# Kernel tuning notes

Hardware: AMD Instinct MI355X
Metric: run time of the kernel (lower is better)

The kernel has to match this reference:

```python
import jax, jax.numpy as jnp
import numpy as np

B, N, C = 4, 1024, 256
E = 65536
HID = 256  # LAYERS = [256, 256, 256]

def _linear_init(key, out_dim, in_dim):
    kw, kb = jax.random.split(key)
    s = 1.0 / np.sqrt(in_dim)
    W = jax.random.uniform(kw, (out_dim, in_dim), jnp.float32, -s, s)
    b = jax.random.uniform(kb, (out_dim,), jnp.float32, -s, s)
    return W, b

def setup_inputs() -> dict:
    key = jax.random.key(0)
    ks = jax.random.split(key, 5)
    pooled_features = jax.random.normal(ks[0], (B, N, C), jnp.float32)
    edge_index = jax.random.randint(ks[1], (2, E), 0, B * N)  # [src; dst]
    W1, b1 = _linear_init(ks[2], HID, 2 * C)
    W2, b2 = _linear_init(ks[3], HID, 2 * HID)
    W3, b3 = _linear_init(ks[4], HID, 2 * HID)
    return {"pooled_features": pooled_features, "edge_index": edge_index,
            "W1": W1, "b1": b1, "W2": W2, "b2": b2, "W3": W3, "b3": b3}

def _edge_conv(x, src, dst, num_nodes, W, b):
    # PyG EdgeConv: x_j = x[src], x_i = x[dst]; msg = relu(fc([x_j - x_i, x_i]));
    # aggr='max' scatters messages onto dst nodes.
    x_i = x[dst]                                   # [E, d]
    x_j = x[src]                                   # [E, d]
    msg = jnp.concatenate([x_j - x_i, x_i], axis=-1)  # [E, 2d]
    msg = jax.nn.relu(msg @ W.T + b)               # [E, out]
    out = jax.ops.segment_max(msg, dst, num_segments=num_nodes)
    # empty segments -> -inf; PyG fills with 0, and relu messages are >= 0
    return jnp.maximum(out, 0.0)

def reference(pooled_features, edge_index, W1, b1, W2, b2, W3, b3):
    b_, n_, c_ = pooled_features.shape
    num_nodes = b_ * n_
    x = pooled_features.reshape(num_nodes, c_)
    src, dst = edge_index[0], edge_index[1]
    feats = [x]
    for W, bb in ((W1, b1), (W2, b2), (W3, b3)):
        x = _edge_conv(x, src, dst, num_nodes, W, bb)
        feats.append(x)
    related_features = jnp.concatenate(feats, axis=-1)  # [num_nodes, 1024]
    return related_features
```

## Files before the change

### kernel.cpp

```cpp
#include <hip/hip_runtime.h>


#define NODES 4096
#define EDGES 65536
#define OSTR 1024
#define DEGCAP 64

typedef __attribute__((ext_vector_type(8))) short bf16x8;
typedef __attribute__((ext_vector_type(4))) float f32x4;

__device__ __forceinline__ unsigned short f2bf(float f) {
    unsigned int x = __float_as_uint(f);
    return (unsigned short)((x + 0x7fff + ((x >> 16) & 1)) >> 16);
}
__device__ __forceinline__ float bf2f(unsigned short u) {
    return __uint_as_float(((unsigned int)u) << 16);
}

__device__ __forceinline__ void gemm_phase(int l, const short* Alds,
                                           const short* __restrict__ Wp,
                                           const float* __restrict__ bias,
                                           unsigned short* __restrict__ UWu,
                                           float* __restrict__ UWw,
                                           int b, int t) {
    const int wv = t >> 6, lane = t & 63;
    const int lm = lane & 15, kq = lane >> 4;
    const int nhalf = wv >> 3, sub = wv & 7;
    f32x4 acc0 = (f32x4){0.f, 0.f, 0.f, 0.f};
    f32x4 acc1 = (f32x4){0.f, 0.f, 0.f, 0.f};
    const short* ap = Alds + lm * 264 + kq * 8;
    const short* bp = Wp + (size_t)l * 131072
                         + (size_t)(nhalf * 256 + sub * 32 + lm) * 256 + kq * 8;
#pragma unroll
    for (int ks = 0; ks < 8; ++ks) {
        const int ko = ks * 32;
        bf16x8 a  = *(const bf16x8*)(ap + ko);
        bf16x8 q0 = *(const bf16x8*)(bp + ko);
        bf16x8 q1 = *(const bf16x8*)(bp + 16 * 256 + ko);
        acc0 = __builtin_amdgcn_mfma_f32_16x16x32_bf16(a, q0, acc0, 0, 0, 0);
        acc1 = __builtin_amdgcn_mfma_f32_16x16x32_bf16(a, q1, acc1, 0, 0, 0);
    }
    unsigned short* UW = UWu + (size_t)(l & 1) * NODES * 256;
#pragma unroll
    for (int nt2 = 0; nt2 < 2; ++nt2) {
        int nc = sub * 32 + nt2 * 16 + lm;
        f32x4 av = nt2 ? acc1 : acc0;
        if (nhalf == 0) {
#pragma unroll
            for (int p = 0; p < 4; ++p)
                UW[(size_t)(b * 16 + kq * 4 + p) * 256 + nc] = f2bf(av[p]);
        } else {
            float bc = bias[nc];
#pragma unroll
            for (int p = 0; p < 4; ++p)
                UWw[(size_t)(b * 16 + kq * 4 + p) * 256 + nc] = av[p] + bc;
        }
    }
}

__device__ __forceinline__ void edge_phase(int l,
                                           const unsigned short* __restrict__ UWu,
                                           const float* __restrict__ UWw,
                                           const int* __restrict__ cursor,
                                           const int* __restrict__ srcS,
                                           float* __restrict__ out,
                                           short* AldsW, int b, int t) {
    const int wv = t >> 6, lane = t & 63;
    const int i = b * 16 + wv;
    int deg = cursor[i]; if (deg > DEGCAP) deg = DEGCAP;
    const int beg = i * DEGCAP, end = beg + deg;
    const unsigned short* UW = UWu + (size_t)(l & 1) * NODES * 256;
    const float NEG = -3.4e38f;
    float mx0 = NEG, mx1 = NEG, mx2 = NEG, mx3 = NEG;
    int e = beg;
    for (; e + 8 <= end; e += 8) {
        int4 sa = *(const int4*)(srcS + e);
        int4 sb = *(const int4*)(srcS + e + 4);
        ushort4 v0 = *(const ushort4*)(UW + (size_t)sa.x * 256 + lane * 4);
        ushort4 v1 = *(const ushort4*)(UW + (size_t)sa.y * 256 + lane * 4);
        ushort4 v2 = *(const ushort4*)(UW + (size_t)sa.z * 256 + lane * 4);
        ushort4 v3 = *(const ushort4*)(UW + (size_t)sa.w * 256 + lane * 4);
        ushort4 v4 = *(const ushort4*)(UW + (size_t)sb.x * 256 + lane * 4);
        ushort4 v5 = *(const ushort4*)(UW + (size_t)sb.y * 256 + lane * 4);
        ushort4 v6 = *(const ushort4*)(UW + (size_t)sb.z * 256 + lane * 4);
        ushort4 v7 = *(const ushort4*)(UW + (size_t)sb.w * 256 + lane * 4);
        mx0 = fmaxf(mx0, fmaxf(fmaxf(bf2f(v0.x), bf2f(v1.x)), fmaxf(bf2f(v2.x), bf2f(v3.x))));
        mx0 = fmaxf(mx0, fmaxf(fmaxf(bf2f(v4.x), bf2f(v5.x)), fmaxf(bf2f(v6.x), bf2f(v7.x))));
        mx1 = fmaxf(mx1, fmaxf(fmaxf(bf2f(v0.y), bf2f(v1.y)), fmaxf(bf2f(v2.y), bf2f(v3.y))));
        mx1 = fmaxf(mx1, fmaxf(fmaxf(bf2f(v4.y), bf2f(v5.y)), fmaxf(bf2f(v6.y), bf2f(v7.y))));
        mx2 = fmaxf(mx2, fmaxf(fmaxf(bf2f(v0.z), bf2f(v1.z)), fmaxf(bf2f(v2.z), bf2f(v3.z))));
        mx2 = fmaxf(mx2, fmaxf(fmaxf(bf2f(v4.z), bf2f(v5.z)), fmaxf(bf2f(v6.z), bf2f(v7.z))));
        mx3 = fmaxf(mx3, fmaxf(fmaxf(bf2f(v0.w), bf2f(v1.w)), fmaxf(bf2f(v2.w), bf2f(v3.w))));
        mx3 = fmaxf(mx3, fmaxf(fmaxf(bf2f(v4.w), bf2f(v5.w)), fmaxf(bf2f(v6.w), bf2f(v7.w))));
    }
    for (; e + 4 <= end; e += 4) {
        int4 sa = *(const int4*)(srcS + e);
        ushort4 v0 = *(const ushort4*)(UW + (size_t)sa.x * 256 + lane * 4);
        ushort4 v1 = *(const ushort4*)(UW + (size_t)sa.y * 256 + lane * 4);
        ushort4 v2 = *(const ushort4*)(UW + (size_t)sa.z * 256 + lane * 4);
        ushort4 v3 = *(const ushort4*)(UW + (size_t)sa.w * 256 + lane * 4);
        mx0 = fmaxf(mx0, fmaxf(fmaxf(bf2f(v0.x), bf2f(v1.x)), fmaxf(bf2f(v2.x), bf2f(v3.x))));
        mx1 = fmaxf(mx1, fmaxf(fmaxf(bf2f(v0.y), bf2f(v1.y)), fmaxf(bf2f(v2.y), bf2f(v3.y))));
        mx2 = fmaxf(mx2, fmaxf(fmaxf(bf2f(v0.z), bf2f(v1.z)), fmaxf(bf2f(v2.z), bf2f(v3.z))));
        mx3 = fmaxf(mx3, fmaxf(fmaxf(bf2f(v0.w), bf2f(v1.w)), fmaxf(bf2f(v2.w), bf2f(v3.w))));
    }
    for (; e < end; ++e) {
        int s = srcS[e];
        ushort4 v = *(const ushort4*)(UW + (size_t)s * 256 + lane * 4);
        mx0 = fmaxf(mx0, bf2f(v.x)); mx1 = fmaxf(mx1, bf2f(v.y));
        mx2 = fmaxf(mx2, bf2f(v.z)); mx3 = fmaxf(mx3, bf2f(v.w));
    }
    float4 w4 = *(const float4*)(UWw + (size_t)i * 256 + lane * 4);
    f32x4 r;
    r[0] = fmaxf(mx0 + w4.x, 0.0f);
    r[1] = fmaxf(mx1 + w4.y, 0.0f);
    r[2] = fmaxf(mx2 + w4.z, 0.0f);
    r[3] = fmaxf(mx3 + w4.w, 0.0f);
    *(f32x4*)(out + (size_t)i * OSTR + (l + 1) * 256 + lane * 4) = r;
    if (AldsW) {
        ushort4 rb;
        rb.x = f2bf(r[0]); rb.y = f2bf(r[1]); rb.z = f2bf(r[2]); rb.w = f2bf(r[3]);
        *(ushort4*)(AldsW + wv * 264 + lane * 4) = rb;
    }
}

__global__ __launch_bounds__(256) void k_prep(const float* __restrict__ W0,
                                              const float* __restrict__ W1,
                                              const float* __restrict__ W2,
                                              short* __restrict__ Wp,
                                              int* __restrict__ cursor) {
    int tid = blockIdx.x * 256 + threadIdx.x;
    const float* Ws[3] = {W0, W1, W2};
#pragma unroll
    for (int layer = 0; layer < 3; ++layer) {
        const float* W = Ws[layer];
        int n2 = tid >> 8, c = tid & 255;
        float wv2 = (n2 < 256) ? W[n2 * 512 + c]
                               : W[(n2 - 256) * 512 + 256 + c] - W[(n2 - 256) * 512 + c];
        Wp[layer * 131072 + tid] = (short)f2bf(wv2);
    }
    if (tid < NODES) cursor[tid] = 0;
}

__global__ __launch_bounds__(1024, 4) void k_g0(const float* __restrict__ x0,
                                                const int* __restrict__ srcIdx,
                                                const int* __restrict__ dstIdx,
                                                const short* __restrict__ Wp,
                                                const float* __restrict__ B0,
                                                unsigned short* __restrict__ UWu,
                                                float* __restrict__ UWw,
                                                int* __restrict__ cursor,
                                                int* __restrict__ srcS,
                                                float* __restrict__ out) {
    __shared__ __align__(16) short Alds[16 * 264];
    const int t = threadIdx.x, b = blockIdx.x;
    const int gtid = b * 1024 + t;
    {
        int row = t >> 6, c4 = t & 63;
        f32x4 v = *((const f32x4*)x0 + (size_t)(b * 16 + row) * 64 + c4);
        ((f32x4*)out)[(size_t)(b * 16 + row) * 256 + c4] = v;
        ushort4 hb;
        hb.x = f2bf(v[0]); hb.y = f2bf(v[1]); hb.z = f2bf(v[2]); hb.w = f2bf(v[3]);
        *(ushort4*)(Alds + row * 264 + c4 * 4) = hb;
    }
    if (gtid < EDGES) {
        int d = dstIdx[gtid];
        int p = atomicAdd(&cursor[d], 1);
        if (p < DEGCAP) srcS[d * DEGCAP + p] = srcIdx[gtid];
    }
    __syncthreads();
    gemm_phase(0, Alds, Wp, B0, UWu, UWw, b, t);
}

__global__ __launch_bounds__(1024, 4) void k_eg(int l,
                                                const short* __restrict__ Wp,
                                                const float* __restrict__ biasN,
                                                unsigned short* __restrict__ UWu,
                                                float* __restrict__ UWw,
                                                const int* __restrict__ cursor,
                                                const int* __restrict__ srcS,
                                                float* __restrict__ out) {
    __shared__ __align__(16) short Alds[16 * 264];
    const int t = threadIdx.x, b = blockIdx.x;
    edge_phase(l, UWu, UWw, cursor, srcS, out, Alds, b, t);
    __syncthreads();
    gemm_phase(l + 1, Alds, Wp, biasN, UWu, UWw, b, t);
}

__global__ __launch_bounds__(1024, 4) void k_e2(const unsigned short* __restrict__ UWu,
                                                const float* __restrict__ UWw,
                                                const int* __restrict__ cursor,
                                                const int* __restrict__ srcS,
                                                float* __restrict__ out) {
    const int t = threadIdx.x, b = blockIdx.x;
    edge_phase(2, UWu, UWw, cursor, srcS, out, (short*)nullptr, b, t);
}

extern "C" void kernel_launch(void* const* d_in, const int* in_sizes, int n_in,
                              void* d_out, int out_size, void* d_ws, size_t ws_size,
                              hipStream_t stream) {
    const float* x0 = (const float*)d_in[0];
    const int* ei = (const int*)d_in[1];
    const int* srcIdx = ei;
    const int* dstIdx = ei + EDGES;
    float* out = (float*)d_out;

    char* w = (char*)d_ws;
    unsigned short* UWu = (unsigned short*)w;
    float* UWw = (float*)(w + 4194304);
    short* Wp = (short*)(w + 8388608);
    int* srcS = (int*)(w + 9175040);
    int* cursor = (int*)(w + 10223616);

    const float* W0 = (const float*)d_in[2]; const float* B0 = (const float*)d_in[3];
    const float* W1 = (const float*)d_in[4]; const float* B1 = (const float*)d_in[5];
    const float* W2 = (const float*)d_in[6]; const float* B2 = (const float*)d_in[7];

    k_prep<<<512, 256, 0, stream>>>(W0, W1, W2, Wp, cursor);
    k_g0<<<256, 1024, 0, stream>>>(x0, srcIdx, dstIdx, Wp, B0, UWu, UWw, cursor, srcS, out);
    k_eg<<<256, 1024, 0, stream>>>(0, Wp, B1, UWu, UWw, cursor, srcS, out);
    k_eg<<<256, 1024, 0, stream>>>(1, Wp, B2, UWu, UWw, cursor, srcS, out);
    k_e2<<<256, 1024, 0, stream>>>(UWu, UWw, cursor, srcS, out);
}
```

Baseline: 131.0 us.

## Fold weight prep into first kernel and bucket edges per block with LDS atomics

Removes the separate prep kernel. Layer-0 weights are now converted straight from fp32 into MFMA B-fragments held in registers, and the layer-1/2 weight packing is spread across k_g0's threads. Edge bucketing changes from global atomics on a cursor array to a per-block scan of all destination indices, using LDS atomics only for the block's own 16 nodes, so the cursor zeroing and its launch go away. The cost is that every block reads the full dst array (64K ints) and holds extra registers for the fragments. The order of sources within each bucket can also change.

```diff
diff --git a/kernel.cpp b/kernel.cpp
--- a/kernel.cpp
+++ b/kernel.cpp
@@ -15,6 +15,14 @@
 }
 __device__ __forceinline__ float bf2f(unsigned short u) {
     return __uint_as_float(((unsigned int)u) << 16);
+}
+__device__ __forceinline__ bf16x8 pack8(float4 a, float4 b) {
+    bf16x8 r;
+    r[0] = (short)f2bf(a.x); r[1] = (short)f2bf(a.y);
+    r[2] = (short)f2bf(a.z); r[3] = (short)f2bf(a.w);
+    r[4] = (short)f2bf(b.x); r[5] = (short)f2bf(b.y);
+    r[6] = (short)f2bf(b.z); r[7] = (short)f2bf(b.w);
+    return r;
 }
 
 __device__ __forceinline__ void gemm_phase(int l, const short* Alds,
@@ -58,16 +66,52 @@
     }
 }
 
+__device__ __forceinline__ void gemm_regs(int par, const bf16x8 fb[2][8],
+                                          const short* Alds,
+                                          const float* __restrict__ bias,
+                                          unsigned short* __restrict__ UWu,
+                                          float* __restrict__ UWw,
+                                          int b, int t) {
+    const int wv = t >> 6, lane = t & 63;
+    const int lm = lane & 15, kq = lane >> 4;
+    const int nhalf = wv >> 3, sub = wv & 7;
+    f32x4 acc0 = (f32x4){0.f, 0.f, 0.f, 0.f};
+    f32x4 acc1 = (f32x4){0.f, 0.f, 0.f, 0.f};
+    const short* ap = Alds + lm * 264 + kq * 8;
+#pragma unroll
+    for (int ks = 0; ks < 8; ++ks) {
+        bf16x8 a = *(const bf16x8*)(ap + ks * 32);
+        acc0 = __builtin_amdgcn_mfma_f32_16x16x32_bf16(a, fb[0][ks], acc0, 0, 0, 0);
+        acc1 = __builtin_amdgcn_mfma_f32_16x16x32_bf16(a, fb[1][ks], acc1, 0, 0, 0);
+    }
+    unsigned short* UW = UWu + (size_t)par * NODES * 256;
+#pragma unroll
+    for (int nt2 = 0; nt2 < 2; ++nt2) {
+        int nc = sub * 32 + nt2 * 16 + lm;
+        f32x4 av = nt2 ? acc1 : acc0;
+        if (nhalf == 0) {
+#pragma unroll
+            for (int p = 0; p < 4; ++p)
+                UW[(size_t)(b * 16 + kq * 4 + p) * 256 + nc] = f2bf(av[p]);
+        } else {
+            float bc = bias[nc];
+#pragma unroll
+            for (int p = 0; p < 4; ++p)
+                UWw[(size_t)(b * 16 + kq * 4 + p) * 256 + nc] = av[p] + bc;
+        }
+    }
+}
+
 __device__ __forceinline__ void edge_phase(int l,
                                            const unsigned short* __restrict__ UWu,
                                            const float* __restrict__ UWw,
-                                           const int* __restrict__ cursor,
+                                           const int* __restrict__ degG,
                                            const int* __restrict__ srcS,
                                            float* __restrict__ out,
                                            short* AldsW, int b, int t) {
     const int wv = t >> 6, lane = t & 63;
     const int i = b * 16 + wv;
-    int deg = cursor[i]; if (deg > DEGCAP) deg = DEGCAP;
+    int deg = degG[i]; if (deg > DEGCAP) deg = DEGCAP;
     const int beg = i * DEGCAP, end = beg + deg;
     const unsigned short* UW = UWu + (size_t)(l & 1) * NODES * 256;
     const float NEG = -3.4e38f;
@@ -124,37 +168,24 @@
     }
 }
 
-__global__ __launch_bounds__(256) void k_prep(const float* __restrict__ W0,
-                                              const float* __restrict__ W1,
-                                              const float* __restrict__ W2,
-                                              short* __restrict__ Wp,
-                                              int* __restrict__ cursor) {
-    int tid = blockIdx.x * 256 + threadIdx.x;
-    const float* Ws[3] = {W0, W1, W2};
-#pragma unroll
-    for (int layer = 0; layer < 3; ++layer) {
-        const float* W = Ws[layer];
-        int n2 = tid >> 8, c = tid & 255;
-        float wv2 = (n2 < 256) ? W[n2 * 512 + c]
-                               : W[(n2 - 256) * 512 + 256 + c] - W[(n2 - 256) * 512 + c];
-        Wp[layer * 131072 + tid] = (short)f2bf(wv2);
-    }
-    if (tid < NODES) cursor[tid] = 0;
-}
-
 __global__ __launch_bounds__(1024, 4) void k_g0(const float* __restrict__ x0,
                                                 const int* __restrict__ srcIdx,
                                                 const int* __restrict__ dstIdx,
-                                                const short* __restrict__ Wp,
+                                                const float* __restrict__ W0,
+                                                const float* __restrict__ W1,
+                                                const float* __restrict__ W2,
                                                 const float* __restrict__ B0,
+                                                short* __restrict__ Wp,
                                                 unsigned short* __restrict__ UWu,
                                                 float* __restrict__ UWw,
-                                                int* __restrict__ cursor,
+                                                int* __restrict__ degG,
                                                 int* __restrict__ srcS,
                                                 float* __restrict__ out) {
     __shared__ __align__(16) short Alds[16 * 264];
+    __shared__ int degL[16];
     const int t = threadIdx.x, b = blockIdx.x;
     const int gtid = b * 1024 + t;
+    if (t < 16) degL[t] = 0;
     {
         int row = t >> 6, c4 = t & 63;
         f32x4 v = *((const f32x4*)x0 + (size_t)(b * 16 + row) * 64 + c4);
@@ -163,13 +194,61 @@
         hb.x = f2bf(v[0]); hb.y = f2bf(v[1]); hb.z = f2bf(v[2]); hb.w = f2bf(v[3]);
         *(ushort4*)(Alds + row * 264 + c4 * 4) = hb;
     }
-    if (gtid < EDGES) {
-        int d = dstIdx[gtid];
-        int p = atomicAdd(&cursor[d], 1);
-        if (p < DEGCAP) srcS[d * DEGCAP + p] = srcIdx[gtid];
+    {
+        const float* W = (gtid >= 131072) ? W2 : W1;
+        int idx = gtid & 131071;
+        int n2 = idx >> 8, c = idx & 255;
+        float wv2 = (n2 < 256) ? W[n2 * 512 + c]
+                               : W[(n2 - 256) * 512 + 256 + c] - W[(n2 - 256) * 512 + c];
+        Wp[131072 + gtid] = (short)f2bf(wv2);
+    }
+    const int wv = t >> 6, lane = t & 63;
+    const int lm = lane & 15, kq = lane >> 4;
+    const int nhalf = wv >> 3, sub = wv & 7;
+    bf16x8 fb[2][8];
+    {
+        const int r0 = sub * 32 + lm;
+#pragma unroll
+        for (int rr = 0; rr < 2; ++rr) {
+            const float* rp = W0 + (size_t)(r0 + rr * 16) * 512 + kq * 8;
+#pragma unroll
+            for (int ks = 0; ks < 8; ++ks) {
+                const int ko = ks * 32;
+                if (nhalf == 0) {
+                    fb[rr][ks] = pack8(*(const float4*)(rp + ko),
+                                       *(const float4*)(rp + ko + 4));
+                } else {
+                    float4 a0 = *(const float4*)(rp + ko);
+                    float4 a1 = *(const float4*)(rp + ko + 4);
+                    float4 c0 = *(const float4*)(rp + 256 + ko);
+                    float4 c1 = *(const float4*)(rp + 256 + ko + 4);
+                    float4 d0, d1;
+                    d0.x = c0.x - a0.x; d0.y = c0.y - a0.y;
+                    d0.z = c0.z - a0.z; d0.w = c0.w - a0.w;
+                    d1.x = c1.x - a1.x; d1.y = c1.y - a1.y;
+                    d1.z = c1.z - a1.z; d1.w = c1.w - a1.w;
+                    fb[rr][ks] = pack8(d0, d1);
+                }
+            }
+        }
     }
     __syncthreads();
-    gemm_phase(0, Alds, Wp, B0, UWu, UWw, b, t);
+#pragma unroll 4
+    for (int j = 0; j < 16; ++j) {
+        int4 dv = ((const int4*)dstIdx)[j * 1024 + t];
+        int e0 = (j * 1024 + t) * 4;
+#pragma unroll
+        for (int k = 0; k < 4; ++k) {
+            int d = (&dv.x)[k];
+            if ((d >> 4) == b) {
+                int p = atomicAdd(&degL[d & 15], 1);
+                if (p < DEGCAP) srcS[d * DEGCAP + p] = srcIdx[e0 + k];
+            }
+        }
+    }
+    __syncthreads();
+    if (t < 16) degG[b * 16 + t] = degL[t];
+    gemm_regs(0, fb, Alds, B0, UWu, UWw, b, t);
 }
 
 __global__ __launch_bounds__(1024, 4) void k_eg(int l,
@@ -177,23 +256,23 @@
                                                 const float* __restrict__ biasN,
                                                 unsigned short* __restrict__ UWu,
                                                 float* __restrict__ UWw,
-                                                const int* __restrict__ cursor,
+                                                const int* __restrict__ degG,
                                                 const int* __restrict__ srcS,
                                                 float* __restrict__ out) {
     __shared__ __align__(16) short Alds[16 * 264];
     const int t = threadIdx.x, b = blockIdx.x;
-    edge_phase(l, UWu, UWw, cursor, srcS, out, Alds, b, t);
+    edge_phase(l, UWu, UWw, degG, srcS, out, Alds, b, t);
     __syncthreads();
     gemm_phase(l + 1, Alds, Wp, biasN, UWu, UWw, b, t);
 }
 
 __global__ __launch_bounds__(1024, 4) void k_e2(const unsigned short* __restrict__ UWu,
                                                 const float* __restrict__ UWw,
-                                                const int* __restrict__ cursor,
+                                                const int* __restrict__ degG,
                                                 const int* __restrict__ srcS,
                                                 float* __restrict__ out) {
     const int t = threadIdx.x, b = blockIdx.x;
-    edge_phase(2, UWu, UWw, cursor, srcS, out, (short*)nullptr, b, t);
+    edge_phase(2, UWu, UWw, degG, srcS, out, (short*)nullptr, b, t);
 }
 
 extern "C" void kernel_launch(void* const* d_in, const int* in_sizes, int n_in,
@@ -210,15 +289,15 @@
     float* UWw = (float*)(w + 4194304);
     short* Wp = (short*)(w + 8388608);
     int* srcS = (int*)(w + 9175040);
-    int* cursor = (int*)(w + 10223616);
+    int* degG = (int*)(w + 10223616);
 
     const float* W0 = (const float*)d_in[2]; const float* B0 = (const float*)d_in[3];
     const float* W1 = (const float*)d_in[4]; const float* B1 = (const float*)d_in[5];
     const float* W2 = (const float*)d_in[6]; const float* B2 = (const float*)d_in[7];
 
-    k_prep<<<512, 256, 0, stream>>>(W0, W1, W2, Wp, cursor);
-    k_g0<<<256, 1024, 0, stream>>>(x0, srcIdx, dstIdx, Wp, B0, UWu, UWw, cursor, srcS, out);
-    k_eg<<<256, 1024, 0, stream>>>(0, Wp, B1, UWu, UWw, cursor, srcS, out);
-    k_eg<<<256, 1024, 0, stream>>>(1, Wp, B2, UWu, UWw, cursor, srcS, out);
-    k_e2<<<256, 1024, 0, stream>>>(UWu, UWw, cursor, srcS, out);
-}
+    k_g0<<<256, 1024, 0, stream>>>(x0, srcIdx, dstIdx, W0, W1, W2, B0,
+                                   Wp, UWu, UWw, degG, srcS, out);
+    k_eg<<<256, 1024, 0, stream>>>(0, Wp, B1, UWu, UWw, degG, srcS, out);
+    k_eg<<<256, 1024, 0, stream>>>(1, Wp, B2, UWu, UWw, degG, srcS, out);
+    k_e2<<<256, 1024, 0, stream>>>(UWu, UWw, degG, srcS, out);
+}
```

New measurement: 149.7 us. +14.2%, slower.
